# Optimization experiments

Measured on AMD Instinct MI355X. Metric: run time of the kernel, lower is better.

Reference implementation:

```python
import jax, jax.numpy as jnp
import numpy as np

B, C, H, W = 8, 512, 64, 64
CR = C // 16  # reduced channels = 32


def setup_inputs() -> dict:
    key = jax.random.key(0)
    ks = jax.random.split(key, 10)
    s_in = 1.0 / np.sqrt(C)
    return {
        "x": jax.random.normal(ks[0], (B, C, H, W), jnp.float32),
        "Wq": jax.random.normal(ks[1], (CR, C), jnp.float32) * s_in,
        "bq": jnp.zeros((CR,), jnp.float32),
        "Wk": jax.random.normal(ks[2], (CR, C), jnp.float32) * s_in,
        "bk": jnp.zeros((CR,), jnp.float32),
        "Wv": jax.random.normal(ks[3], (C, C), jnp.float32) * s_in,
        "bv": jnp.zeros((C,), jnp.float32),
        "Wo": jax.random.normal(ks[4], (C, C), jnp.float32) * s_in,
        "bo": jnp.zeros((C,), jnp.float32),
        "gamma": jax.random.normal(ks[5], (1,), jnp.float32) * 0.1,
    }


def reference(x, Wq, bq, Wk, bk, Wv, bv, Wo, bo, gamma):
    b, c, h, w = x.shape
    n = h * w
    xf = x.reshape(b, c, n)  # [B,C,N]; 1x1 conv == channel matmul
    q = jnp.einsum('rc,bcn->bnr', Wq, xf) + bq  # [B,N,Cr]
    k = jnp.einsum('rc,bcn->brn', Wk, xf) + bk[None, :, None]  # [B,Cr,N]
    v = jnp.einsum('oc,bcn->bon', Wv, xf) + bv[None, :, None]  # [B,C,N]
    attn = jax.nn.softmax(jnp.einsum('bnr,brm->bnm', q, k), axis=-1)  # [B,N,N]
    out = jnp.einsum('bcm,bnm->bcn', v, attn)  # value @ attn^T -> [B,C,N]
    out = jnp.einsum('oc,bcn->bon', Wo, out) + bo[None, :, None]
    out = out.reshape(b, c, h, w)
    return gamma * out + x
```

## Files before the change

kernel.cpp:

```cpp
#include <hip/hip_runtime.h>
#include <stdint.h>

typedef unsigned short u16;
typedef float f32x4 __attribute__((ext_vector_type(4)));
typedef short short8 __attribute__((ext_vector_type(8)));

__device__ __forceinline__ u16 f2bf(float f) {
  union { float f; uint32_t u; } v; v.f = f;
  return (u16)((v.u + 0x7FFFu + ((v.u >> 16) & 1u)) >> 16);
}
__device__ __forceinline__ uint32_t pack2(u16 lo, u16 hi) {
  return (uint32_t)lo | ((uint32_t)hi << 16);
}
__device__ __forceinline__ void gld_lds16(const void* gsrc, void* ldst) {
  __builtin_amdgcn_global_load_lds(
      (const __attribute__((address_space(1))) unsigned int*)gsrc,
      (__attribute__((address_space(3))) unsigned int*)ldst, 16, 0, 0);
}

#define MFMA16(a, b, c) __builtin_amdgcn_mfma_f32_16x16x32_bf16((a), (b), (c), 0, 0, 0)

__global__ void conv_w(const float* __restrict__ src, u16* __restrict__ dst, int n4) {
  int i = blockIdx.x * blockDim.x + threadIdx.x;
  if (i >= n4) return;
  float4 v = ((const float4*)src)[i];
  uint2 p;
  p.x = pack2(f2bf(v.x), f2bf(v.y));
  p.y = pack2(f2bf(v.z), f2bf(v.w));
  ((uint2*)dst)[i] = p;
}

__global__ void conv_wqk(const float* __restrict__ Wq, const float* __restrict__ Wk,
                         u16* __restrict__ dst) {
  int i = blockIdx.x * blockDim.x + threadIdx.x;
  if (i >= 8192) return;
  const float LOG2E = 1.4426950408889634f;
  bool isQ = i < 4096;
  float4 v = isQ ? ((const float4*)Wq)[i] : ((const float4*)Wk)[i - 4096];
  float s = isQ ? LOG2E : 1.0f;
  uint2 p;
  p.x = pack2(f2bf(v.x * s), f2bf(v.y * s));
  p.y = pack2(f2bf(v.z * s), f2bf(v.w * s));
  ((uint2*)dst)[i] = p;
}

__global__ __launch_bounds__(256) void qkv_proj(
    const float* __restrict__ x, const u16* __restrict__ Wvb,
    const u16* __restrict__ Wqkb, const float* __restrict__ bv,
    const float* __restrict__ bq, const float* __restrict__ bk,
    u16* __restrict__ V2, u16* __restrict__ Qb, u16* __restrict__ Kb) {
  const int b = blockIdx.y, nb = blockIdx.x * 64;
  const int t = threadIdx.x, w = t >> 6, lane = t & 63, g = lane >> 4, l15 = lane & 15;
  const int wo = (w >> 1) * 32, wn = (w & 1) * 32;
  __shared__ __align__(16) u16 xT[64][64];

  f32x4 zero4 = {0.f, 0.f, 0.f, 0.f};
  f32x4 acc[8][2][2];
#pragma unroll
  for (int og = 0; og < 8; ++og)
#pragma unroll
    for (int ot = 0; ot < 2; ++ot)
#pragma unroll
      for (int nt = 0; nt < 2; ++nt) acc[og][ot][nt] = zero4;
  f32x4 accq[2][2];
  accq[0][0] = zero4; accq[0][1] = zero4; accq[1][0] = zero4; accq[1][1] = zero4;

  const int cq4 = (t >> 4) * 4, n4 = (t & 15) * 4;

  for (int c0 = 0; c0 < 512; c0 += 64) {
    float4 q0 = *(const float4*)&x[((size_t)(b * 512 + c0 + cq4 + 0)) * 4096 + nb + n4];
    float4 q1 = *(const float4*)&x[((size_t)(b * 512 + c0 + cq4 + 1)) * 4096 + nb + n4];
    float4 q2 = *(const float4*)&x[((size_t)(b * 512 + c0 + cq4 + 2)) * 4096 + nb + n4];
    float4 q3 = *(const float4*)&x[((size_t)(b * 512 + c0 + cq4 + 3)) * 4096 + nb + n4];
    float rr[4][4];
    rr[0][0] = q0.x; rr[0][1] = q0.y; rr[0][2] = q0.z; rr[0][3] = q0.w;
    rr[1][0] = q1.x; rr[1][1] = q1.y; rr[1][2] = q1.z; rr[1][3] = q1.w;
    rr[2][0] = q2.x; rr[2][1] = q2.y; rr[2][2] = q2.z; rr[2][3] = q2.w;
    rr[3][0] = q3.x; rr[3][1] = q3.y; rr[3][2] = q3.z; rr[3][3] = q3.w;
#pragma unroll
    for (int k = 0; k < 4; ++k) {
      int row = n4 + k;
      uint2 pk;
      pk.x = pack2(f2bf(rr[0][k]), f2bf(rr[1][k]));
      pk.y = pack2(f2bf(rr[2][k]), f2bf(rr[3][k]));
      int byte = row * 128 + ((cq4 * 2) ^ ((row & 7) << 4));
      *(uint2*)((char*)&xT[0][0] + byte) = pk;
    }
    __syncthreads();

    short8 bb[2][2];
#pragma unroll
    for (int nt = 0; nt < 2; ++nt)
#pragma unroll
      for (int ks = 0; ks < 2; ++ks) {
        int row = wn + nt * 16 + l15;
        int byte = row * 128 + (((ks * 64) + (g * 16)) ^ ((row & 7) << 4));
        bb[nt][ks] = *(const short8*)((const char*)&xT[0][0] + byte);
      }
#pragma unroll
    for (int og = 0; og < 8; ++og) {
      short8 af[2][2];
#pragma unroll
      for (int ot = 0; ot < 2; ++ot)
#pragma unroll
        for (int ks = 0; ks < 2; ++ks)
          af[ot][ks] = *(const short8*)&Wvb[(size_t)(og * 64 + wo + ot * 16 + l15) * 512 + c0 + ks * 32 + g * 8];
#pragma unroll
      for (int ks = 0; ks < 2; ++ks)
#pragma unroll
        for (int ot = 0; ot < 2; ++ot)
#pragma unroll
          for (int nt = 0; nt < 2; ++nt)
            acc[og][ot][nt] = MFMA16(af[ot][ks], bb[nt][ks], acc[og][ot][nt]);
    }
    {
      short8 aq[2][2];
#pragma unroll
      for (int ot = 0; ot < 2; ++ot)
#pragma unroll
        for (int ks = 0; ks < 2; ++ks)
          aq[ot][ks] = *(const short8*)&Wqkb[(size_t)(wo + ot * 16 + l15) * 512 + c0 + ks * 32 + g * 8];
#pragma unroll
      for (int ks = 0; ks < 2; ++ks)
#pragma unroll
        for (int ot = 0; ot < 2; ++ot)
#pragma unroll
          for (int nt = 0; nt < 2; ++nt)
            accq[ot][nt] = MFMA16(aq[ot][ks], bb[nt][ks], accq[ot][nt]);
    }
    __syncthreads();
  }

  const size_t tbase = (size_t)b * 2097152 + (size_t)(nb >> 6) * 32768;
#pragma unroll
  for (int og = 0; og < 8; ++og)
#pragma unroll
    for (int ot = 0; ot < 2; ++ot)
#pragma unroll
      for (int nt = 0; nt < 2; ++nt)
#pragma unroll
        for (int r = 0; r < 4; ++r) {
          int o = og * 64 + wo + ot * 16 + g * 4 + r;
          int kk = wn + nt * 16 + l15;
          int swz = ((kk * 2) ^ ((o & 7) << 4)) >> 1;
          V2[tbase + o * 64 + swz] = f2bf(acc[og][ot][nt][r] + bv[o]);
        }
  const float LOG2E = 1.4426950408889634f;
#pragma unroll
  for (int ot = 0; ot < 2; ++ot)
#pragma unroll
    for (int nt = 0; nt < 2; ++nt)
#pragma unroll
      for (int r = 0; r < 4; ++r) {
        int o = wo + ot * 16 + g * 4 + r;
        int n = nb + wn + nt * 16 + l15;
        if (o < 32) {
          Qb[((size_t)(b * 4096 + n)) * 32 + o] = f2bf(accq[ot][nt][r] + bq[o] * LOG2E);
        } else {
          Kb[((size_t)(b * 4096 + n)) * 32 + (o - 32)] = f2bf(accq[ot][nt][r] + bk[o - 32]);
        }
      }
}

__global__ __launch_bounds__(512, 1) void attn_f(
    const u16* __restrict__ Qb, const u16* __restrict__ Kb,
    const u16* __restrict__ V2, const u16* __restrict__ Wob,
    const float* __restrict__ bo, const float* __restrict__ gamma,
    const float* __restrict__ x, float* __restrict__ out) {
  const int bid = blockIdx.x;
  const int b = bid & 7;
  const int qblk = (bid >> 3) * 128;
  const int t = threadIdx.x;
  const int w = t >> 6, lane = t & 63, g = lane >> 4, l15 = lane & 15;
  const int qg = w & 3, chh = w >> 2;
  const int qbase = qblk + qg * 32;
  const int chb = chh * 256;

  __shared__ __align__(16) u16 Vlds[2][32768];
  __shared__ __align__(16) u16 Plds[4][32][88];
  __shared__ float lsum[4][32];

  f32x4 zero4 = {0.f, 0.f, 0.f, 0.f};

  short8 qf[2];
  if (chh == 0) {
#pragma unroll
    for (int qt = 0; qt < 2; ++qt)
      qf[qt] = *(const short8*)&Qb[((size_t)(b * 4096 + qbase + qt * 16 + l15)) * 32 + g * 8];
  }

  f32x4 acc[2][16];
#pragma unroll
  for (int qt = 0; qt < 2; ++qt)
#pragma unroll
    for (int ct = 0; ct < 16; ++ct) acc[qt][ct] = zero4;
  float l_[2][4] = {{0.f, 0.f, 0.f, 0.f}, {0.f, 0.f, 0.f, 0.f}};

  const char* VBb = (const char*)(V2 + (size_t)b * 2097152);
  const size_t kb0 = (size_t)b * 4096;

  {
    const char* gsrc = VBb + w * 8192 + lane * 16;
    char* ldst = (char*)&Vlds[0][0] + w * 8192;
#pragma unroll
    for (int j = 0; j < 8; ++j) gld_lds16(gsrc + j * 1024, ldst + j * 1024);
  }
  if (chh == 0) {
    float rsv[2][4];
#pragma unroll
    for (int half = 0; half < 2; ++half) {
      short8 kfA = *(const short8*)&Kb[(kb0 + 0 + half * 32 + 0 + l15) * 32 + g * 8];
      short8 kfB = *(const short8*)&Kb[(kb0 + 0 + half * 32 + 16 + l15) * 32 + g * 8];
      f32x4 sA[2], sB[2];
      sA[0] = MFMA16(qf[0], kfA, zero4); sA[1] = MFMA16(qf[1], kfA, zero4);
      sB[0] = MFMA16(qf[0], kfB, zero4); sB[1] = MFMA16(qf[1], kfB, zero4);
#pragma unroll
      for (int qt = 0; qt < 2; ++qt)
#pragma unroll
        for (int r = 0; r < 4; ++r) {
          float pA = exp2f(sA[qt][r]), pB = exp2f(sB[qt][r]);
          Plds[qg][qt * 16 + g * 4 + r][(half * 2 + 0) * 16 + l15] = f2bf(pA);
          Plds[qg][qt * 16 + g * 4 + r][(half * 2 + 1) * 16 + l15] = f2bf(pB);
          float v = pA + pB;
          rsv[qt][r] = half ? (rsv[qt][r] + v) : v;
        }
    }
#pragma unroll
    for (int qt = 0; qt < 2; ++qt)
#pragma unroll
      for (int r = 0; r < 4; ++r) {
        float rs = rsv[qt][r];
        rs += __shfl_xor(rs, 1);
        rs += __shfl_xor(rs, 2);
        rs += __shfl_xor(rs, 4);
        rs += __shfl_xor(rs, 8);
        l_[qt][r] += rs;
      }
  }
  asm volatile("s_waitcnt vmcnt(0) lgkmcnt(0)" ::: "memory");
  __builtin_amdgcn_s_barrier();
  __builtin_amdgcn_sched_barrier(0);

  for (int kv = 0; kv < 4096; kv += 64) {
    const int buf = (kv >> 6) & 1;
    const bool more = (kv + 64) < 4096;

    if (more) {
      const char* gsrc = VBb + (size_t)((kv >> 6) + 1) * 65536 + w * 8192 + lane * 16;
      char* ldst = (char*)&Vlds[buf ^ 1][0] + w * 8192;
#pragma unroll
      for (int j = 0; j < 8; ++j) gld_lds16(gsrc + j * 1024, ldst + j * 1024);
    }

    short8 pf[2][2];
#pragma unroll
    for (int qt = 0; qt < 2; ++qt)
#pragma unroll
      for (int k2 = 0; k2 < 2; ++k2)
        pf[qt][k2] = *(const short8*)&Plds[qg][qt * 16 + l15][k2 * 32 + g * 8];

    asm volatile("s_waitcnt lgkmcnt(0)" ::: "memory");
    __builtin_amdgcn_s_barrier();
    __builtin_amdgcn_sched_barrier(0);

    if (chh == 0 && more) {
      float rsv[2][4];
#pragma unroll
      for (int half = 0; half < 2; ++half) {
        short8 kfA = *(const short8*)&Kb[(kb0 + kv + 64 + half * 32 + 0 + l15) * 32 + g * 8];
        short8 kfB = *(const short8*)&Kb[(kb0 + kv + 64 + half * 32 + 16 + l15) * 32 + g * 8];
        f32x4 sA[2], sB[2];
        sA[0] = MFMA16(qf[0], kfA, zero4); sA[1] = MFMA16(qf[1], kfA, zero4);
        sB[0] = MFMA16(qf[0], kfB, zero4); sB[1] = MFMA16(qf[1], kfB, zero4);
#pragma unroll
        for (int qt = 0; qt < 2; ++qt)
#pragma unroll
          for (int r = 0; r < 4; ++r) {
            float pA = exp2f(sA[qt][r]), pB = exp2f(sB[qt][r]);
            Plds[qg][qt * 16 + g * 4 + r][(half * 2 + 0) * 16 + l15] = f2bf(pA);
            Plds[qg][qt * 16 + g * 4 + r][(half * 2 + 1) * 16 + l15] = f2bf(pB);
            float v = pA + pB;
            rsv[qt][r] = half ? (rsv[qt][r] + v) : v;
          }
      }
#pragma unroll
      for (int qt = 0; qt < 2; ++qt)
#pragma unroll
        for (int r = 0; r < 4; ++r) {
          float rs = rsv[qt][r];
          rs += __shfl_xor(rs, 1);
          rs += __shfl_xor(rs, 2);
          rs += __shfl_xor(rs, 4);
          rs += __shfl_xor(rs, 8);
          l_[qt][r] += rs;
        }
    }

#pragma unroll
    for (int ct = 0; ct < 16; ++ct) {
      int c = chb + ct * 16 + l15;
      int sw = (c & 7) << 4;
      const char* vrow = (const char*)&Vlds[buf][0] + c * 128;
      short8 vf0 = *(const short8*)(vrow + ((g * 16) ^ sw));
      short8 vf1 = *(const short8*)(vrow + ((64 + g * 16) ^ sw));
      acc[0][ct] = MFMA16(pf[0][0], vf0, acc[0][ct]);
      acc[0][ct] = MFMA16(pf[0][1], vf1, acc[0][ct]);
      acc[1][ct] = MFMA16(pf[1][0], vf0, acc[1][ct]);
      acc[1][ct] = MFMA16(pf[1][1], vf1, acc[1][ct]);
    }

    asm volatile("s_waitcnt vmcnt(0) lgkmcnt(0)" ::: "memory");
    __builtin_amdgcn_s_barrier();
    __builtin_amdgcn_sched_barrier(0);
  }

  if (chh == 0 && l15 == 0) {
#pragma unroll
    for (int qt = 0; qt < 2; ++qt)
#pragma unroll
      for (int r = 0; r < 4; ++r)
        lsum[qg][qt * 16 + g * 4 + r] = l_[qt][r];
  }
  __syncthreads();

  u16* AO = (u16*)&Vlds[0][0];
#pragma unroll
  for (int qt = 0; qt < 2; ++qt) {
    float inv[4];
#pragma unroll
    for (int r = 0; r < 4; ++r) inv[r] = 1.0f / lsum[qg][qt * 16 + g * 4 + r];
#pragma unroll
    for (int ct = 0; ct < 16; ++ct)
#pragma unroll
      for (int r = 0; r < 4; ++r) {
        int nrow = qg * 32 + qt * 16 + g * 4 + r;
        int c = chb + ct * 16 + l15;
        AO[nrow * 512 + (c ^ ((nrow & 7) << 3))] = f2bf(acc[qt][ct][r] * inv[r]);
      }
  }
  __syncthreads();

  f32x4 oacc[4][8];
#pragma unroll
  for (int ot = 0; ot < 4; ++ot)
#pragma unroll
    for (int nt = 0; nt < 8; ++nt) oacc[ot][nt] = zero4;

  for (int c0 = 0; c0 < 512; c0 += 64) {
#pragma unroll
    for (int nth = 0; nth < 2; ++nth) {
      short8 bb[4][2];
#pragma unroll
      for (int n2 = 0; n2 < 4; ++n2)
#pragma unroll
        for (int ks = 0; ks < 2; ++ks) {
          int row = (nth * 4 + n2) * 16 + l15;
          int coff = (c0 + ks * 32 + g * 8) ^ ((row & 7) << 3);
          bb[n2][ks] = *(const short8*)&AO[row * 512 + coff];
        }
#pragma unroll
      for (int ot = 0; ot < 4; ++ot) {
        short8 af[2];
#pragma unroll
        for (int ks = 0; ks < 2; ++ks)
          af[ks] = *(const short8*)&Wob[(size_t)(w * 64 + ot * 16 + l15) * 512 + c0 + ks * 32 + g * 8];
#pragma unroll
        for (int ks = 0; ks < 2; ++ks)
#pragma unroll
          for (int n2 = 0; n2 < 4; ++n2)
            oacc[ot][nth * 4 + n2] = MFMA16(af[ks], bb[n2][ks], oacc[ot][nth * 4 + n2]);
      }
    }
  }

  float gm = gamma[0];
#pragma unroll
  for (int ot = 0; ot < 4; ++ot)
#pragma unroll
    for (int nt = 0; nt < 8; ++nt)
#pragma unroll
      for (int r = 0; r < 4; ++r) {
        int o = w * 64 + ot * 16 + g * 4 + r;
        int n = qblk + nt * 16 + l15;
        size_t idx = ((size_t)(b * 512 + o)) * 4096 + n;
        out[idx] = gm * (oacc[ot][nt][r] + bo[o]) + x[idx];
      }
}

extern "C" void kernel_launch(void* const* d_in, const int* in_sizes, int n_in,
                              void* d_out, int out_size, void* d_ws, size_t ws_size,
                              hipStream_t stream) {
  (void)in_sizes; (void)n_in; (void)out_size; (void)ws_size;
  const float* x     = (const float*)d_in[0];
  const float* Wq    = (const float*)d_in[1];
  const float* bq    = (const float*)d_in[2];
  const float* Wk    = (const float*)d_in[3];
  const float* bk    = (const float*)d_in[4];
  const float* Wv    = (const float*)d_in[5];
  const float* bv    = (const float*)d_in[6];
  const float* Wo    = (const float*)d_in[7];
  const float* bo    = (const float*)d_in[8];
  const float* gamma = (const float*)d_in[9];

  char* wsb = (char*)d_ws;
  u16* V2   = (u16*)(wsb + 0);
  u16* Qb   = (u16*)(wsb + (size_t)33554432);
  u16* Kb   = (u16*)(wsb + (size_t)35651584);
  u16* Wvb  = (u16*)(wsb + (size_t)37748736);
  u16* Wob  = (u16*)(wsb + (size_t)38273024);
  u16* Wqkb = (u16*)(wsb + (size_t)38797312);

  conv_w<<<256, 256, 0, stream>>>(Wv, Wvb, 65536);
  conv_w<<<256, 256, 0, stream>>>(Wo, Wob, 65536);
  conv_wqk<<<32, 256, 0, stream>>>(Wq, Wk, Wqkb);
  qkv_proj<<<dim3(64, 8), 256, 0, stream>>>(x, Wvb, Wqkb, bv, bq, bk, V2, Qb, Kb);
  attn_f<<<256, 512, 0, stream>>>(Qb, Kb, V2, Wob, bo, gamma, x, (float*)d_out);
}
```

Baseline: 387.8 us.

## Rebalance attention waves to 64x128 tiles and share QK/softmax across all waves

In the attention kernel, each wave now owns 64 query rows by 128 channels instead of 32 rows by 256 channels. The QK^T score and exp computation is split across all 8 waves, each handling a 16-key slice, instead of being done only by the four waves with chh==0. Row sums are combined from four partial lsum slices at the end, and the next K fragment load is issued early. The projection kernel also register-double-buffers its x loads so the next channel block is fetched during the current block's MFMAs; this raises register pressure with the fully unrolled loop.

```diff
diff --git a/kernel.cpp b/kernel.cpp
--- a/kernel.cpp
+++ b/kernel.cpp
@@ -66,17 +66,28 @@
   accq[0][0] = zero4; accq[0][1] = zero4; accq[1][0] = zero4; accq[1][1] = zero4;
 
   const int cq4 = (t >> 4) * 4, n4 = (t & 15) * 4;
-
-  for (int c0 = 0; c0 < 512; c0 += 64) {
-    float4 q0 = *(const float4*)&x[((size_t)(b * 512 + c0 + cq4 + 0)) * 4096 + nb + n4];
-    float4 q1 = *(const float4*)&x[((size_t)(b * 512 + c0 + cq4 + 1)) * 4096 + nb + n4];
-    float4 q2 = *(const float4*)&x[((size_t)(b * 512 + c0 + cq4 + 2)) * 4096 + nb + n4];
-    float4 q3 = *(const float4*)&x[((size_t)(b * 512 + c0 + cq4 + 3)) * 4096 + nb + n4];
+  const size_t xrow = (size_t)(b * 512) * 4096 + nb + n4;
+
+  float4 cur0 = *(const float4*)&x[xrow + (size_t)(cq4 + 0) * 4096];
+  float4 cur1 = *(const float4*)&x[xrow + (size_t)(cq4 + 1) * 4096];
+  float4 cur2 = *(const float4*)&x[xrow + (size_t)(cq4 + 2) * 4096];
+  float4 cur3 = *(const float4*)&x[xrow + (size_t)(cq4 + 3) * 4096];
+
+#pragma unroll
+  for (int ci = 0; ci < 8; ++ci) {
+    const int c0 = ci * 64;
+    float4 nxt0, nxt1, nxt2, nxt3;
+    if (ci < 7) {
+      nxt0 = *(const float4*)&x[xrow + (size_t)(c0 + 64 + cq4 + 0) * 4096];
+      nxt1 = *(const float4*)&x[xrow + (size_t)(c0 + 64 + cq4 + 1) * 4096];
+      nxt2 = *(const float4*)&x[xrow + (size_t)(c0 + 64 + cq4 + 2) * 4096];
+      nxt3 = *(const float4*)&x[xrow + (size_t)(c0 + 64 + cq4 + 3) * 4096];
+    }
     float rr[4][4];
-    rr[0][0] = q0.x; rr[0][1] = q0.y; rr[0][2] = q0.z; rr[0][3] = q0.w;
-    rr[1][0] = q1.x; rr[1][1] = q1.y; rr[1][2] = q1.z; rr[1][3] = q1.w;
-    rr[2][0] = q2.x; rr[2][1] = q2.y; rr[2][2] = q2.z; rr[2][3] = q2.w;
-    rr[3][0] = q3.x; rr[3][1] = q3.y; rr[3][2] = q3.z; rr[3][3] = q3.w;
+    rr[0][0] = cur0.x; rr[0][1] = cur0.y; rr[0][2] = cur0.z; rr[0][3] = cur0.w;
+    rr[1][0] = cur1.x; rr[1][1] = cur1.y; rr[1][2] = cur1.z; rr[1][3] = cur1.w;
+    rr[2][0] = cur2.x; rr[2][1] = cur2.y; rr[2][2] = cur2.z; rr[2][3] = cur2.w;
+    rr[3][0] = cur3.x; rr[3][1] = cur3.y; rr[3][2] = cur3.z; rr[3][3] = cur3.w;
 #pragma unroll
     for (int k = 0; k < 4; ++k) {
       int row = n4 + k;
@@ -129,6 +140,7 @@
             accq[ot][nt] = MFMA16(aq[ot][ks], bb[nt][ks], accq[ot][nt]);
     }
     __syncthreads();
+    if (ci < 7) { cur0 = nxt0; cur1 = nxt1; cur2 = nxt2; cur3 = nxt3; }
   }
 
   const size_t tbase = (size_t)b * 2097152 + (size_t)(nb >> 6) * 32768;
@@ -172,29 +184,31 @@
   const int qblk = (bid >> 3) * 128;
   const int t = threadIdx.x;
   const int w = t >> 6, lane = t & 63, g = lane >> 4, l15 = lane & 15;
-  const int qg = w & 3, chh = w >> 2;
-  const int qbase = qblk + qg * 32;
-  const int chb = chh * 256;
+  const int qh = w & 1, cq = w >> 1;
+  const int qbase = qblk + qh * 64;
+  const int chb = cq * 128;
 
   __shared__ __align__(16) u16 Vlds[2][32768];
-  __shared__ __align__(16) u16 Plds[4][32][88];
-  __shared__ float lsum[4][32];
+  __shared__ __align__(16) u16 Plds[2][64][88];
+  __shared__ float lsum[2][4][64];
 
   f32x4 zero4 = {0.f, 0.f, 0.f, 0.f};
 
-  short8 qf[2];
-  if (chh == 0) {
-#pragma unroll
-    for (int qt = 0; qt < 2; ++qt)
-      qf[qt] = *(const short8*)&Qb[((size_t)(b * 4096 + qbase + qt * 16 + l15)) * 32 + g * 8];
-  }
-
-  f32x4 acc[2][16];
-#pragma unroll
-  for (int qt = 0; qt < 2; ++qt)
-#pragma unroll
-    for (int ct = 0; ct < 16; ++ct) acc[qt][ct] = zero4;
-  float l_[2][4] = {{0.f, 0.f, 0.f, 0.f}, {0.f, 0.f, 0.f, 0.f}};
+  short8 qf[4];
+#pragma unroll
+  for (int qt = 0; qt < 4; ++qt)
+    qf[qt] = *(const short8*)&Qb[((size_t)(b * 4096 + qbase + qt * 16 + l15)) * 32 + g * 8];
+
+  f32x4 acc[4][8];
+#pragma unroll
+  for (int qt = 0; qt < 4; ++qt)
+#pragma unroll
+    for (int ct = 0; ct < 8; ++ct) acc[qt][ct] = zero4;
+  float l_[4][4];
+#pragma unroll
+  for (int qt = 0; qt < 4; ++qt)
+#pragma unroll
+    for (int r = 0; r < 4; ++r) l_[qt][r] = 0.f;
 
   const char* VBb = (const char*)(V2 + (size_t)b * 2097152);
   const size_t kb0 = (size_t)b * 4096;
@@ -205,31 +219,18 @@
 #pragma unroll
     for (int j = 0; j < 8; ++j) gld_lds16(gsrc + j * 1024, ldst + j * 1024);
   }
-  if (chh == 0) {
-    float rsv[2][4];
-#pragma unroll
-    for (int half = 0; half < 2; ++half) {
-      short8 kfA = *(const short8*)&Kb[(kb0 + 0 + half * 32 + 0 + l15) * 32 + g * 8];
-      short8 kfB = *(const short8*)&Kb[(kb0 + 0 + half * 32 + 16 + l15) * 32 + g * 8];
-      f32x4 sA[2], sB[2];
-      sA[0] = MFMA16(qf[0], kfA, zero4); sA[1] = MFMA16(qf[1], kfA, zero4);
-      sB[0] = MFMA16(qf[0], kfB, zero4); sB[1] = MFMA16(qf[1], kfB, zero4);
-#pragma unroll
-      for (int qt = 0; qt < 2; ++qt)
-#pragma unroll
-        for (int r = 0; r < 4; ++r) {
-          float pA = exp2f(sA[qt][r]), pB = exp2f(sB[qt][r]);
-          Plds[qg][qt * 16 + g * 4 + r][(half * 2 + 0) * 16 + l15] = f2bf(pA);
-          Plds[qg][qt * 16 + g * 4 + r][(half * 2 + 1) * 16 + l15] = f2bf(pB);
-          float v = pA + pB;
-          rsv[qt][r] = half ? (rsv[qt][r] + v) : v;
-        }
-    }
-#pragma unroll
-    for (int qt = 0; qt < 2; ++qt)
+  {
+    short8 kf = *(const short8*)&Kb[(kb0 + 0 + cq * 16 + l15) * 32 + g * 8];
+    f32x4 s[4];
+#pragma unroll
+    for (int qt = 0; qt < 4; ++qt) s[qt] = MFMA16(qf[qt], kf, zero4);
+#pragma unroll
+    for (int qt = 0; qt < 4; ++qt)
 #pragma unroll
       for (int r = 0; r < 4; ++r) {
-        float rs = rsv[qt][r];
+        float p = exp2f(s[qt][r]);
+        Plds[qh][qt * 16 + g * 4 + r][cq * 16 + l15] = f2bf(p);
+        float rs = p;
         rs += __shfl_xor(rs, 1);
         rs += __shfl_xor(rs, 2);
         rs += __shfl_xor(rs, 4);
@@ -251,43 +252,32 @@
 #pragma unroll
       for (int j = 0; j < 8; ++j) gld_lds16(gsrc + j * 1024, ldst + j * 1024);
     }
-
-    short8 pf[2][2];
-#pragma unroll
-    for (int qt = 0; qt < 2; ++qt)
+    short8 kfn;
+    if (more)
+      kfn = *(const short8*)&Kb[(kb0 + kv + 64 + cq * 16 + l15) * 32 + g * 8];
+
+    short8 pf[4][2];
+#pragma unroll
+    for (int qt = 0; qt < 4; ++qt)
 #pragma unroll
       for (int k2 = 0; k2 < 2; ++k2)
-        pf[qt][k2] = *(const short8*)&Plds[qg][qt * 16 + l15][k2 * 32 + g * 8];
+        pf[qt][k2] = *(const short8*)&Plds[qh][qt * 16 + l15][k2 * 32 + g * 8];
 
     asm volatile("s_waitcnt lgkmcnt(0)" ::: "memory");
     __builtin_amdgcn_s_barrier();
     __builtin_amdgcn_sched_barrier(0);
 
-    if (chh == 0 && more) {
-      float rsv[2][4];
-#pragma unroll
-      for (int half = 0; half < 2; ++half) {
-        short8 kfA = *(const short8*)&Kb[(kb0 + kv + 64 + half * 32 + 0 + l15) * 32 + g * 8];
-        short8 kfB = *(const short8*)&Kb[(kb0 + kv + 64 + half * 32 + 16 + l15) * 32 + g * 8];
-        f32x4 sA[2], sB[2];
-        sA[0] = MFMA16(qf[0], kfA, zero4); sA[1] = MFMA16(qf[1], kfA, zero4);
-        sB[0] = MFMA16(qf[0], kfB, zero4); sB[1] = MFMA16(qf[1], kfB, zero4);
-#pragma unroll
-        for (int qt = 0; qt < 2; ++qt)
-#pragma unroll
-          for (int r = 0; r < 4; ++r) {
-            float pA = exp2f(sA[qt][r]), pB = exp2f(sB[qt][r]);
-            Plds[qg][qt * 16 + g * 4 + r][(half * 2 + 0) * 16 + l15] = f2bf(pA);
-            Plds[qg][qt * 16 + g * 4 + r][(half * 2 + 1) * 16 + l15] = f2bf(pB);
-            float v = pA + pB;
-            rsv[qt][r] = half ? (rsv[qt][r] + v) : v;
-          }
-      }
-#pragma unroll
-      for (int qt = 0; qt < 2; ++qt)
+    if (more) {
+      f32x4 s[4];
+#pragma unroll
+      for (int qt = 0; qt < 4; ++qt) s[qt] = MFMA16(qf[qt], kfn, zero4);
+#pragma unroll
+      for (int qt = 0; qt < 4; ++qt)
 #pragma unroll
         for (int r = 0; r < 4; ++r) {
-          float rs = rsv[qt][r];
+          float p = exp2f(s[qt][r]);
+          Plds[qh][qt * 16 + g * 4 + r][cq * 16 + l15] = f2bf(p);
+          float rs = p;
           rs += __shfl_xor(rs, 1);
           rs += __shfl_xor(rs, 2);
           rs += __shfl_xor(rs, 4);
@@ -297,16 +287,17 @@
     }
 
 #pragma unroll
-    for (int ct = 0; ct < 16; ++ct) {
+    for (int ct = 0; ct < 8; ++ct) {
       int c = chb + ct * 16 + l15;
       int sw = (c & 7) << 4;
       const char* vrow = (const char*)&Vlds[buf][0] + c * 128;
       short8 vf0 = *(const short8*)(vrow + ((g * 16) ^ sw));
       short8 vf1 = *(const short8*)(vrow + ((64 + g * 16) ^ sw));
-      acc[0][ct] = MFMA16(pf[0][0], vf0, acc[0][ct]);
-      acc[0][ct] = MFMA16(pf[0][1], vf1, acc[0][ct]);
-      acc[1][ct] = MFMA16(pf[1][0], vf0, acc[1][ct]);
-      acc[1][ct] = MFMA16(pf[1][1], vf1, acc[1][ct]);
+#pragma unroll
+      for (int qt = 0; qt < 4; ++qt) {
+        acc[qt][ct] = MFMA16(pf[qt][0], vf0, acc[qt][ct]);
+        acc[qt][ct] = MFMA16(pf[qt][1], vf1, acc[qt][ct]);
+      }
     }
 
     asm volatile("s_waitcnt vmcnt(0) lgkmcnt(0)" ::: "memory");
@@ -314,26 +305,30 @@
     __builtin_amdgcn_sched_barrier(0);
   }
 
-  if (chh == 0 && l15 == 0) {
-#pragma unroll
-    for (int qt = 0; qt < 2; ++qt)
+  if (l15 == 0) {
+#pragma unroll
+    for (int qt = 0; qt < 4; ++qt)
 #pragma unroll
       for (int r = 0; r < 4; ++r)
-        lsum[qg][qt * 16 + g * 4 + r] = l_[qt][r];
+        lsum[qh][cq][qt * 16 + g * 4 + r] = l_[qt][r];
   }
   __syncthreads();
 
   u16* AO = (u16*)&Vlds[0][0];
 #pragma unroll
-  for (int qt = 0; qt < 2; ++qt) {
+  for (int qt = 0; qt < 4; ++qt) {
     float inv[4];
 #pragma unroll
-    for (int r = 0; r < 4; ++r) inv[r] = 1.0f / lsum[qg][qt * 16 + g * 4 + r];
-#pragma unroll
-    for (int ct = 0; ct < 16; ++ct)
+    for (int r = 0; r < 4; ++r) {
+      int row = qt * 16 + g * 4 + r;
+      inv[r] = 1.0f / ((lsum[qh][0][row] + lsum[qh][1][row]) +
+                       (lsum[qh][2][row] + lsum[qh][3][row]));
+    }
+#pragma unroll
+    for (int ct = 0; ct < 8; ++ct)
 #pragma unroll
       for (int r = 0; r < 4; ++r) {
-        int nrow = qg * 32 + qt * 16 + g * 4 + r;
+        int nrow = qh * 64 + qt * 16 + g * 4 + r;
         int c = chb + ct * 16 + l15;
         AO[nrow * 512 + (c ^ ((nrow & 7) << 3))] = f2bf(acc[qt][ct][r] * inv[r]);
       }
```

Measured after the change: 363.5 us. -6.3%, faster.

## Double attention block to 16 waves and prefetch x in projection

Applied to the files above, without the earlier changes.

The attention kernel now launches 1024 threads, so each wave owns 128 output channels instead of 256 and 32 output-projection rows instead of 64. This halves per-wave accumulators and gives more waves to hide latency. The QKV projection kernel now prefetches the next x channel slab into registers while the current one is processed. The score/softmax step is recast into four 16-key slices, each doing its own row-sum shuffle reduction, which adds shuffles. The aggressive launch bound could squeeze register allocation and cause spills.

```diff
diff --git a/kernel.cpp b/kernel.cpp
--- a/kernel.cpp
+++ b/kernel.cpp
@@ -66,17 +66,28 @@
   accq[0][0] = zero4; accq[0][1] = zero4; accq[1][0] = zero4; accq[1][1] = zero4;
 
   const int cq4 = (t >> 4) * 4, n4 = (t & 15) * 4;
-
-  for (int c0 = 0; c0 < 512; c0 += 64) {
-    float4 q0 = *(const float4*)&x[((size_t)(b * 512 + c0 + cq4 + 0)) * 4096 + nb + n4];
-    float4 q1 = *(const float4*)&x[((size_t)(b * 512 + c0 + cq4 + 1)) * 4096 + nb + n4];
-    float4 q2 = *(const float4*)&x[((size_t)(b * 512 + c0 + cq4 + 2)) * 4096 + nb + n4];
-    float4 q3 = *(const float4*)&x[((size_t)(b * 512 + c0 + cq4 + 3)) * 4096 + nb + n4];
+  const size_t xrow = (size_t)(b * 512) * 4096 + nb + n4;
+
+  float4 cur0 = *(const float4*)&x[xrow + (size_t)(cq4 + 0) * 4096];
+  float4 cur1 = *(const float4*)&x[xrow + (size_t)(cq4 + 1) * 4096];
+  float4 cur2 = *(const float4*)&x[xrow + (size_t)(cq4 + 2) * 4096];
+  float4 cur3 = *(const float4*)&x[xrow + (size_t)(cq4 + 3) * 4096];
+
+#pragma unroll
+  for (int ci = 0; ci < 8; ++ci) {
+    const int c0 = ci * 64;
+    float4 nxt0, nxt1, nxt2, nxt3;
+    if (ci < 7) {
+      nxt0 = *(const float4*)&x[xrow + (size_t)(c0 + 64 + cq4 + 0) * 4096];
+      nxt1 = *(const float4*)&x[xrow + (size_t)(c0 + 64 + cq4 + 1) * 4096];
+      nxt2 = *(const float4*)&x[xrow + (size_t)(c0 + 64 + cq4 + 2) * 4096];
+      nxt3 = *(const float4*)&x[xrow + (size_t)(c0 + 64 + cq4 + 3) * 4096];
+    }
     float rr[4][4];
-    rr[0][0] = q0.x; rr[0][1] = q0.y; rr[0][2] = q0.z; rr[0][3] = q0.w;
-    rr[1][0] = q1.x; rr[1][1] = q1.y; rr[1][2] = q1.z; rr[1][3] = q1.w;
-    rr[2][0] = q2.x; rr[2][1] = q2.y; rr[2][2] = q2.z; rr[2][3] = q2.w;
-    rr[3][0] = q3.x; rr[3][1] = q3.y; rr[3][2] = q3.z; rr[3][3] = q3.w;
+    rr[0][0] = cur0.x; rr[0][1] = cur0.y; rr[0][2] = cur0.z; rr[0][3] = cur0.w;
+    rr[1][0] = cur1.x; rr[1][1] = cur1.y; rr[1][2] = cur1.z; rr[1][3] = cur1.w;
+    rr[2][0] = cur2.x; rr[2][1] = cur2.y; rr[2][2] = cur2.z; rr[2][3] = cur2.w;
+    rr[3][0] = cur3.x; rr[3][1] = cur3.y; rr[3][2] = cur3.z; rr[3][3] = cur3.w;
 #pragma unroll
     for (int k = 0; k < 4; ++k) {
       int row = n4 + k;
@@ -129,6 +140,7 @@
             accq[ot][nt] = MFMA16(aq[ot][ks], bb[nt][ks], accq[ot][nt]);
     }
     __syncthreads();
+    if (ci < 7) { cur0 = nxt0; cur1 = nxt1; cur2 = nxt2; cur3 = nxt3; }
   }
 
   const size_t tbase = (size_t)b * 2097152 + (size_t)(nb >> 6) * 32768;
@@ -162,7 +174,7 @@
       }
 }
 
-__global__ __launch_bounds__(512, 1) void attn_f(
+__global__ __launch_bounds__(1024, 4) void attn_f(
     const u16* __restrict__ Qb, const u16* __restrict__ Kb,
     const u16* __restrict__ V2, const u16* __restrict__ Wob,
     const float* __restrict__ bo, const float* __restrict__ gamma,
@@ -174,7 +186,7 @@
   const int w = t >> 6, lane = t & 63, g = lane >> 4, l15 = lane & 15;
   const int qg = w & 3, chh = w >> 2;
   const int qbase = qblk + qg * 32;
-  const int chb = chh * 256;
+  const int chb = chh * 128;
 
   __shared__ __align__(16) u16 Vlds[2][32768];
   __shared__ __align__(16) u16 Plds[4][32][88];
@@ -189,105 +201,35 @@
       qf[qt] = *(const short8*)&Qb[((size_t)(b * 4096 + qbase + qt * 16 + l15)) * 32 + g * 8];
   }
 
-  f32x4 acc[2][16];
+  f32x4 acc[2][8];
 #pragma unroll
   for (int qt = 0; qt < 2; ++qt)
 #pragma unroll
-    for (int ct = 0; ct < 16; ++ct) acc[qt][ct] = zero4;
+    for (int ct = 0; ct < 8; ++ct) acc[qt][ct] = zero4;
   float l_[2][4] = {{0.f, 0.f, 0.f, 0.f}, {0.f, 0.f, 0.f, 0.f}};
 
   const char* VBb = (const char*)(V2 + (size_t)b * 2097152);
   const size_t kb0 = (size_t)b * 4096;
 
   {
-    const char* gsrc = VBb + w * 8192 + lane * 16;
-    char* ldst = (char*)&Vlds[0][0] + w * 8192;
-#pragma unroll
-    for (int j = 0; j < 8; ++j) gld_lds16(gsrc + j * 1024, ldst + j * 1024);
+    const char* gsrc = VBb + w * 4096 + lane * 16;
+    char* ldst = (char*)&Vlds[0][0] + w * 4096;
+#pragma unroll
+    for (int j = 0; j < 4; ++j) gld_lds16(gsrc + j * 1024, ldst + j * 1024);
   }
   if (chh == 0) {
-    float rsv[2][4];
-#pragma unroll
-    for (int half = 0; half < 2; ++half) {
-      short8 kfA = *(const short8*)&Kb[(kb0 + 0 + half * 32 + 0 + l15) * 32 + g * 8];
-      short8 kfB = *(const short8*)&Kb[(kb0 + 0 + half * 32 + 16 + l15) * 32 + g * 8];
-      f32x4 sA[2], sB[2];
-      sA[0] = MFMA16(qf[0], kfA, zero4); sA[1] = MFMA16(qf[1], kfA, zero4);
-      sB[0] = MFMA16(qf[0], kfB, zero4); sB[1] = MFMA16(qf[1], kfB, zero4);
+#pragma unroll
+    for (int sl = 0; sl < 4; ++sl) {
+      short8 kf = *(const short8*)&Kb[(kb0 + 0 + sl * 16 + l15) * 32 + g * 8];
+      f32x4 s0 = MFMA16(qf[0], kf, zero4);
+      f32x4 s1 = MFMA16(qf[1], kf, zero4);
 #pragma unroll
       for (int qt = 0; qt < 2; ++qt)
 #pragma unroll
         for (int r = 0; r < 4; ++r) {
-          float pA = exp2f(sA[qt][r]), pB = exp2f(sB[qt][r]);
-          Plds[qg][qt * 16 + g * 4 + r][(half * 2 + 0) * 16 + l15] = f2bf(pA);
-          Plds[qg][qt * 16 + g * 4 + r][(half * 2 + 1) * 16 + l15] = f2bf(pB);
-          float v = pA + pB;
-          rsv[qt][r] = half ? (rsv[qt][r] + v) : v;
-        }
-    }
-#pragma unroll
-    for (int qt = 0; qt < 2; ++qt)
-#pragma unroll
-      for (int r = 0; r < 4; ++r) {
-        float rs = rsv[qt][r];
-        rs += __shfl_xor(rs, 1);
-        rs += __shfl_xor(rs, 2);
-        rs += __shfl_xor(rs, 4);
-        rs += __shfl_xor(rs, 8);
-        l_[qt][r] += rs;
-      }
-  }
-  asm volatile("s_waitcnt vmcnt(0) lgkmcnt(0)" ::: "memory");
-  __builtin_amdgcn_s_barrier();
-  __builtin_amdgcn_sched_barrier(0);
-
-  for (int kv = 0; kv < 4096; kv += 64) {
-    const int buf = (kv >> 6) & 1;
-    const bool more = (kv + 64) < 4096;
-
-    if (more) {
-      const char* gsrc = VBb + (size_t)((kv >> 6) + 1) * 65536 + w * 8192 + lane * 16;
-      char* ldst = (char*)&Vlds[buf ^ 1][0] + w * 8192;
-#pragma unroll
-      for (int j = 0; j < 8; ++j) gld_lds16(gsrc + j * 1024, ldst + j * 1024);
-    }
-
-    short8 pf[2][2];
-#pragma unroll
-    for (int qt = 0; qt < 2; ++qt)
-#pragma unroll
-      for (int k2 = 0; k2 < 2; ++k2)
-        pf[qt][k2] = *(const short8*)&Plds[qg][qt * 16 + l15][k2 * 32 + g * 8];
-
-    asm volatile("s_waitcnt lgkmcnt(0)" ::: "memory");
-    __builtin_amdgcn_s_barrier();
-    __builtin_amdgcn_sched_barrier(0);
-
-    if (chh == 0 && more) {
-      float rsv[2][4];
-#pragma unroll
-      for (int half = 0; half < 2; ++half) {
-        short8 kfA = *(const short8*)&Kb[(kb0 + kv + 64 + half * 32 + 0 + l15) * 32 + g * 8];
-        short8 kfB = *(const short8*)&Kb[(kb0 + kv + 64 + half * 32 + 16 + l15) * 32 + g * 8];
-        f32x4 sA[2], sB[2];
-        sA[0] = MFMA16(qf[0], kfA, zero4); sA[1] = MFMA16(qf[1], kfA, zero4);
-        sB[0] = MFMA16(qf[0], kfB, zero4); sB[1] = MFMA16(qf[1], kfB, zero4);
-#pragma unroll
-        for (int qt = 0; qt < 2; ++qt)
-#pragma unroll
-          for (int r = 0; r < 4; ++r) {
-            float pA = exp2f(sA[qt][r]), pB = exp2f(sB[qt][r]);
-            Plds[qg][qt * 16 + g * 4 + r][(half * 2 + 0) * 16 + l15] = f2bf(pA);
-            Plds[qg][qt * 16 + g * 4 + r][(half * 2 + 1) * 16 + l15] = f2bf(pB);
-            float v = pA + pB;
-            rsv[qt][r] = half ? (rsv[qt][r] + v) : v;
-          }
-      }
-#pragma unroll
-      for (int qt = 0; qt < 2; ++qt)
-#pragma unroll
-        for (int r = 0; r < 4; ++r) {
-          float rs = rsv[qt][r];
+          float p = exp2f(qt ? s1[r] : s0[r]);
+          Plds[qg][qt * 16 + g * 4 + r][sl * 16 + l15] = f2bf(p);
+          float rs = p;
           rs += __shfl_xor(rs, 1);
           rs += __shfl_xor(rs, 2);
           rs += __shfl_xor(rs, 4);
@@ -295,9 +237,57 @@
           l_[qt][r] += rs;
         }
     }
-
-#pragma unroll
-    for (int ct = 0; ct < 16; ++ct) {
+  }
+  asm volatile("s_waitcnt vmcnt(0) lgkmcnt(0)" ::: "memory");
+  __builtin_amdgcn_s_barrier();
+  __builtin_amdgcn_sched_barrier(0);
+
+  for (int kv = 0; kv < 4096; kv += 64) {
+    const int buf = (kv >> 6) & 1;
+    const bool more = (kv + 64) < 4096;
+
+    if (more) {
+      const char* gsrc = VBb + (size_t)((kv >> 6) + 1) * 65536 + w * 4096 + lane * 16;
+      char* ldst = (char*)&Vlds[buf ^ 1][0] + w * 4096;
+#pragma unroll
+      for (int j = 0; j < 4; ++j) gld_lds16(gsrc + j * 1024, ldst + j * 1024);
+    }
+
+    short8 pf[2][2];
+#pragma unroll
+    for (int qt = 0; qt < 2; ++qt)
+#pragma unroll
+      for (int k2 = 0; k2 < 2; ++k2)
+        pf[qt][k2] = *(const short8*)&Plds[qg][qt * 16 + l15][k2 * 32 + g * 8];
+
+    asm volatile("s_waitcnt lgkmcnt(0)" ::: "memory");
+    __builtin_amdgcn_s_barrier();
+    __builtin_amdgcn_sched_barrier(0);
+
+    if (chh == 0 && more) {
+#pragma unroll
+      for (int sl = 0; sl < 4; ++sl) {
+        short8 kf = *(const short8*)&Kb[(kb0 + kv + 64 + sl * 16 + l15) * 32 + g * 8];
+        f32x4 s0 = MFMA16(qf[0], kf, zero4);
+        f32x4 s1 = MFMA16(qf[1], kf, zero4);
+#pragma unroll
+        for (int qt = 0; qt < 2; ++qt)
+#pragma unroll
+          for (int r = 0; r < 4; ++r) {
+            float p = exp2f(qt ? s1[r] : s0[r]);
+            Plds[qg][qt * 16 + g * 4 + r][sl * 16 + l15] = f2bf(p);
+            float rs = p;
+            rs += __shfl_xor(rs, 1);
+            rs += __shfl_xor(rs, 2);
+            rs += __shfl_xor(rs, 4);
+            rs += __shfl_xor(rs, 8);
+            l_[qt][r] += rs;
+          }
+      }
+    }
+
+#pragma unroll
+    for (int ct = 0; ct < 8; ++ct) {
       int c = chb + ct * 16 + l15;
       int sw = (c & 7) << 4;
       const char* vrow = (const char*)&Vlds[buf][0] + c * 128;
@@ -330,7 +320,7 @@
 #pragma unroll
     for (int r = 0; r < 4; ++r) inv[r] = 1.0f / lsum[qg][qt * 16 + g * 4 + r];
 #pragma unroll
-    for (int ct = 0; ct < 16; ++ct)
+    for (int ct = 0; ct < 8; ++ct)
 #pragma unroll
       for (int r = 0; r < 4; ++r) {
         int nrow = qg * 32 + qt * 16 + g * 4 + r;
@@ -340,9 +330,9 @@
   }
   __syncthreads();
 
-  f32x4 oacc[4][8];
-#pragma unroll
-  for (int ot = 0; ot < 4; ++ot)
+  f32x4 oacc[2][8];
+#pragma unroll
+  for (int ot = 0; ot < 2; ++ot)
 #pragma unroll
     for (int nt = 0; nt < 8; ++nt) oacc[ot][nt] = zero4;
 
@@ -359,11 +349,11 @@
           bb[n2][ks] = *(const short8*)&AO[row * 512 + coff];
         }
 #pragma unroll
-      for (int ot = 0; ot < 4; ++ot) {
+      for (int ot = 0; ot < 2; ++ot) {
         short8 af[2];
 #pragma unroll
         for (int ks = 0; ks < 2; ++ks)
-          af[ks] = *(const short8*)&Wob[(size_t)(w * 64 + ot * 16 + l15) * 512 + c0 + ks * 32 + g * 8];
+          af[ks] = *(const short8*)&Wob[(size_t)(w * 32 + ot * 16 + l15) * 512 + c0 + ks * 32 + g * 8];
 #pragma unroll
         for (int ks = 0; ks < 2; ++ks)
 #pragma unroll
@@ -375,12 +365,12 @@
 
   float gm = gamma[0];
 #pragma unroll
-  for (int ot = 0; ot < 4; ++ot)
+  for (int ot = 0; ot < 2; ++ot)
 #pragma unroll
     for (int nt = 0; nt < 8; ++nt)
 #pragma unroll
       for (int r = 0; r < 4; ++r) {
-        int o = w * 64 + ot * 16 + g * 4 + r;
+        int o = w * 32 + ot * 16 + g * 4 + r;
         int n = qblk + nt * 16 + l15;
         size_t idx = ((size_t)(b * 512 + o)) * 4096 + n;
         out[idx] = gm * (oacc[ot][nt][r] + bo[o]) + x[idx];
@@ -414,5 +404,5 @@
   conv_w<<<256, 256, 0, stream>>>(Wo, Wob, 65536);
   conv_wqk<<<32, 256, 0, stream>>>(Wq, Wk, Wqkb);
   qkv_proj<<<dim3(64, 8), 256, 0, stream>>>(x, Wvb, Wqkb, bv, bq, bk, V2, Qb, Kb);
-  attn_f<<<256, 512, 0, stream>>>(Qb, Kb, V2, Wob, bo, gamma, x, (float*)d_out);
-}
+  attn_f<<<256, 1024, 0, stream>>>(Qb, Kb, V2, Wob, bo, gamma, x, (float*)d_out);
+}
```

Measured after the change: 488.8 us. 26.0% more time.
